# Optimization experiments

Measured on AMD Instinct MI355X. Metric: run time of the kernel, lower is better.

Reference implementation:

```python
import jax, jax.numpy as jnp
import numpy as np

B, LATENT, P, NUM_ATOMS, H, L, E = 16, 128, 16, 64, 64, 4, 32768
N = P * NUM_ATOMS  # 1024

def _lin(k, i, o, s=0.05):
    kw, kb = jax.random.split(k)
    return jax.random.normal(kw, (i, o), jnp.float32) * s, jax.random.normal(kb, (o,), jnp.float32) * s

def setup_inputs() -> dict:
    key = jax.random.key(0)
    ks = jax.random.split(key, 32)
    z = jax.random.normal(ks[0], (B, LATENT), jnp.float32)
    edge_index = jax.random.randint(ks[1], (2, E), 0, N, jnp.int32)
    # build_node_features: (frame/P, atom/num_atoms, 1) per node
    fr = jnp.repeat(jnp.arange(P), NUM_ATOMS) / P
    at = jnp.tile(jnp.arange(NUM_ATOMS), P) / NUM_ATOMS
    node_features = jnp.stack([fr, at, jnp.ones(N)], -1).astype(jnp.float32)
    Wg, bg = _lin(ks[2], LATENT, H)
    Wn, bn = _lin(ks[3], 3, H)
    def stack(fn, base):
        outs = [fn(jax.random.fold_in(key, base + l)) for l in range(L)]
        return tuple(jnp.stack(t) for t in zip(*outs))
    eW1, eb1 = stack(lambda k: _lin(k, 2 * H + 1, H), 100)
    eW2, eb2 = stack(lambda k: _lin(k, H, H), 200)
    cW1, cb1 = stack(lambda k: _lin(k, H, H), 300)
    cW2 = jnp.stack([jax.random.normal(jax.random.fold_in(key, 400 + l), (H, 1), jnp.float32) * 0.05 for l in range(L)])
    nW1, nb1 = stack(lambda k: _lin(k, 2 * H, H), 500)
    nW2, nb2 = stack(lambda k: _lin(k, H, H), 600)
    lng = jnp.ones((L, H), jnp.float32)
    lnb = jnp.zeros((L, H), jnp.float32)
    oW1, ob1 = _lin(ks[4], H, H)
    oW2, ob2 = _lin(ks[5], H, 3)
    return dict(z=z, edge_index=edge_index, node_features=node_features, Wg=Wg, bg=bg, Wn=Wn, bn=bn,
                eW1=eW1, eb1=eb1, eW2=eW2, eb2=eb2, cW1=cW1, cb1=cb1, cW2=cW2,
                nW1=nW1, nb1=nb1, nW2=nW2, nb2=nb2, lng=lng, lnb=lnb,
                oW1=oW1, ob1=ob1, oW2=oW2, ob2=ob2)

def _forward(z, edge_index, node_features, Wg, bg, Wn, bn, eW1, eb1, eW2, eb2,
             cW1, cb1, cW2, nW1, nb1, nW2, nb2, lng, lnb, oW1, ob1, oW2, ob2):
    b = z.shape[0]
    n = node_features.shape[0]
    row, col = edge_index[0], edge_index[1]  # aggregate messages to row
    counts = jnp.clip(jnp.zeros((n,), jnp.float32).at[row].add(1.0), 1.0, None)
    g = z @ Wg + bg                              # [B,H]
    h = (node_features @ Wn + bn)[None] + g[:, None]  # [B,N,H]
    pos = jnp.zeros((b, n, 3), h.dtype)
    for l in range(L):
        hi, hj = h[:, row], h[:, col]            # [B,E,H] gathers
        diff = pos[:, row] - pos[:, col]         # [B,E,3]
        d2 = jnp.sum(diff * diff, -1, keepdims=True)
        m = jax.nn.silu(jnp.concatenate([hi, hj, d2], -1) @ eW1[l] + eb1[l])
        m = jax.nn.silu(m @ eW2[l] + eb2[l])     # [B,E,H]
        w = jax.nn.silu(m @ cW1[l] + cb1[l]) @ cW2[l]  # [B,E,1]
        trans = diff * w
        pos = pos + jnp.zeros_like(pos).at[:, row].add(trans) / counts[None, :, None]
        agg = jnp.zeros_like(h).at[:, row].add(m)      # scatter-sum to nodes
        u = jax.nn.silu(jnp.concatenate([h, agg], -1) @ nW1[l] + nb1[l]) @ nW2[l] + nb2[l]
        h = h + u                                 # node residual
        mu = jnp.mean(h, -1, keepdims=True)
        var = jnp.mean((h - mu) ** 2, -1, keepdims=True)
        h = (h - mu) * jax.lax.rsqrt(var + 1e-5) * lng[l] + lnb[l]
    out = jax.nn.relu(h @ oW1 + ob1) @ oW2 + ob2   # [B,N,3]
    return out.reshape(b, -1)

def reference(z, edge_index, node_features, Wg, bg, Wn, bn, eW1, eb1, eW2, eb2,
              cW1, cb1, cW2, nW1, nb1, nW2, nb2, lng, lnb, oW1, ob1, oW2, ob2):
    return _forward(z, edge_index, node_features, Wg, bg, Wn, bn, eW1, eb1, eW2, eb2,
                    cW1, cb1, cW2, nW1, nb1, nW2, nb2, lng, lnb, oW1, ob1, oW2, ob2)
```

## Files before the change

kernel.cpp:

```cpp
#include <hip/hip_runtime.h>
#include <hip/hip_bf16.h>


namespace {

constexpr int kB = 16, kN = 1024, kH = 64, kE = 32768, kLat = 128;
constexpr int kC = 24;
constexpr int kMaxItems = 2560;

typedef __attribute__((ext_vector_type(8))) short short8;
typedef __attribute__((ext_vector_type(4))) float floatx4;

__device__ __forceinline__ unsigned short f2bf(float f){
  union { float f; unsigned int u; } v; v.f = f;
  unsigned int r = v.u + 0x7fffu + ((v.u >> 16) & 1u);
  return (unsigned short)(r >> 16);
}
__device__ __forceinline__ unsigned int packbf(float a, float b){
  return ((unsigned int)f2bf(b) << 16) | (unsigned int)f2bf(a);
}
__device__ __forceinline__ unsigned int pack2f(float a, float b){
  unsigned int ua = __float_as_uint(a) + 0x8000u;
  unsigned int ub = __float_as_uint(b) + 0x8000u;
  return __builtin_amdgcn_perm(ub, ua, 0x07060302);
}
__device__ __forceinline__ float bflo(unsigned int u){
  union { unsigned int u; float f; } v; v.u = u << 16; return v.f;
}
__device__ __forceinline__ float bfhi(unsigned int u){
  union { unsigned int u; float f; } v; v.u = u & 0xffff0000u; return v.f;
}
__device__ __forceinline__ float silu2(float x){
  float u = __builtin_amdgcn_exp2f(-1.44269504f * x);
  return x * __builtin_amdgcn_rcpf(1.0f + u);
}

__global__ void k_count(const int* ei, int* cntI){
  int e = blockIdx.x*256 + threadIdx.x;
  atomicAdd(&cntI[ei[e]], 1);
}

__global__ void k_scan(const int* cntI, int* off, int* ioff, int* fill,
                       int* items, int* nitems){
  __shared__ int s0[1024];
  __shared__ int s1[1024];
  int t = threadIdx.x;
  int c = cntI[t];
  s0[t] = c; __syncthreads();
  int* src = s0; int* dst = s1;
  for (int o = 1; o < 1024; o <<= 1){
    int v = src[t] + ((t >= o) ? src[t-o] : 0);
    dst[t] = v; __syncthreads();
    int* tmp = src; src = dst; dst = tmp;
  }
  int inc = src[t];
  off[t] = inc - c;
  if (t == 1023) off[1024] = inc;
  fill[t] = 0;
  int ic = (c + (kC-1)) / kC;
  __syncthreads();
  s0[t] = ic; __syncthreads();
  src = s0; dst = s1;
  for (int o = 1; o < 1024; o <<= 1){
    int v = src[t] + ((t >= o) ? src[t-o] : 0);
    dst[t] = v; __syncthreads();
    int* tmp = src; src = dst; dst = tmp;
  }
  int inc2 = src[t];
  int ib = inc2 - ic;
  ioff[t] = ib;
  if (t == 1023){ ioff[1024] = inc2; *nitems = inc2; }
  for (int s = 0; s < ic; s++) items[ib + s] = (t << 12) | s;
}

__global__ void k_bucket(const int* ei, const int* off, int* fill, int* ecol,
                         const float* eW2, unsigned short* wfragE,
                         const float* z, const float* Wg, const float* bg,
                         float* g){
  int e = blockIdx.x*256 + threadIdx.x;
  int r = ei[e];
  int s = atomicAdd(&fill[r], 1);
  ecol[off[r] + s] = ei[kE + e];
  if (blockIdx.x < 4){
    int l = blockIdx.x;
    for (int i = threadIdx.x; i < 4096; i += 256){
      int f = i >> 9, lane = (i >> 3) & 63, j8 = i & 7;
      int jt = f >> 1, ks = f & 1;
      int k = ks*32 + (lane >> 4)*8 + j8;
      int j = jt*16 + (lane & 15);
      wfragE[l*4096 + i] = f2bf(eW2[l*4096 + k*64 + j]);
    }
  } else if (blockIdx.x < 8){
    int b = (blockIdx.x - 4)*4 + (threadIdx.x >> 6);
    int j = threadIdx.x & 63;
    float acc = bg[j];
    for (int k = 0; k < kLat; k++) acc += z[b*kLat + k] * Wg[k*64 + j];
    g[b*64 + j] = acc;
  }
}

__global__ __launch_bounds__(256, 3) void k_pre(const float* nf, const float* Wn,
      const float* bn, const float* g, const float* eW1, const float* eb1,
      float* h, float* A1t, unsigned short* A2bf){
  __shared__ __align__(16) float W0[4096];
  __shared__ __align__(16) float W1[4096];
  __shared__ __align__(16) float HR[16*68];
  __shared__ float b1s[64];
  int tid = threadIdx.x;
  int bb = blockIdx.x >> 6;
  int n0 = (blockIdx.x & 63) * 16;
  {
    const float4* e1a = (const float4*)(eW1);
    const float4* e1b = (const float4*)(eW1 + 4096);
    for (int i = tid; i < 1024; i += 256){ ((float4*)W0)[i] = e1a[i]; ((float4*)W1)[i] = e1b[i]; }
  }
  if (tid < 64) b1s[tid] = eb1[tid];
  int rl = tid >> 4, c = tid & 15, j0 = c*4;
  int n = n0 + rl;
  int row = bb*1024 + n;
  float f0 = nf[n*3], f1 = nf[n*3+1], f2 = nf[n*3+2];
  float4 hv;
  hv.x = f0*Wn[j0+0] + f1*Wn[64+j0+0] + f2*Wn[128+j0+0] + bn[j0+0] + g[bb*64+j0+0];
  hv.y = f0*Wn[j0+1] + f1*Wn[64+j0+1] + f2*Wn[128+j0+1] + bn[j0+1] + g[bb*64+j0+1];
  hv.z = f0*Wn[j0+2] + f1*Wn[64+j0+2] + f2*Wn[128+j0+2] + bn[j0+2] + g[bb*64+j0+2];
  hv.w = f0*Wn[j0+3] + f1*Wn[64+j0+3] + f2*Wn[128+j0+3] + bn[j0+3] + g[bb*64+j0+3];
  *(float4*)(h + row*64 + j0) = hv;
  *(float4*)(HR + rl*68 + j0) = hv;
  __syncthreads();
  float4 a1 = { b1s[j0], b1s[j0+1], b1s[j0+2], b1s[j0+3] };
  float4 a2 = { 0.f, 0.f, 0.f, 0.f };
  #pragma unroll 8
  for (int k = 0; k < 64; k++){
    float hk = HR[rl*68 + k];
    float4 w1 = *(const float4*)(W0 + k*64 + j0);
    float4 w2 = *(const float4*)(W1 + k*64 + j0);
    a1.x += hk*w1.x; a1.y += hk*w1.y; a1.z += hk*w1.z; a1.w += hk*w1.w;
    a2.x += hk*w2.x; a2.y += hk*w2.y; a2.z += hk*w2.z; a2.w += hk*w2.w;
  }
  int tb = (n*16 + bb)*64;
  *(float4*)(A1t + tb + j0) = a1;
  uint2 pk; pk.x = packbf(a2.x, a2.y); pk.y = packbf(a2.z, a2.w);
  *(uint2*)(A2bf + tb + j0) = pk;
}

__global__ __launch_bounds__(256, 3) void k_edge(const float* A1t,
      const unsigned short* A2bf, const unsigned short* wfragE,
      const float* eb2, int l, const int* off, const int* ecol,
      const int* items, const int* nitems, float* P){
  int w = blockIdx.x*4 + (threadIdx.x >> 6);
  if (w >= *nitems) return;
  int lane = threadIdx.x & 63;
  int m = lane & 15, quad = lane >> 4;
  int it = items[w];
  int r = it >> 12, s = it & 4095;
  int e0 = off[r] + s*kC;
  int e1 = min(off[r+1], e0 + kC);

  short8 wf[8];
  #pragma unroll
  for (int f = 0; f < 8; f++)
    wf[f] = *(const short8*)(wfragE + l*4096 + f*512 + lane*8);

  float4 a1[4];
  #pragma unroll
  for (int ks = 0; ks < 2; ks++){
    a1[ks*2+0] = *(const float4*)(A1t + (r<<10) + (m<<6) + ks*32 + quad*8);
    a1[ks*2+1] = *(const float4*)(A1t + (r<<10) + (m<<6) + ks*32 + quad*8 + 4);
  }
  floatx4 dini[4];
  #pragma unroll
  for (int jt = 0; jt < 4; jt++)
    dini[jt] = *(const floatx4*)(eb2 + l*64 + jt*16 + quad*4);
  floatx4 agg[4];
  #pragma unroll
  for (int jt = 0; jt < 4; jt++) agg[jt] = (floatx4){0.f,0.f,0.f,0.f};

  int c0 = ecol[e0];
  uint4 p0 = *(const uint4*)(A2bf + ((c0<<4)+m)*64 + quad*8);
  uint4 p1 = *(const uint4*)(A2bf + ((c0<<4)+m)*64 + 32 + quad*8);

  for (int e = e0; e < e1; e++){
    uint4 c_0 = p0, c_1 = p1;
    if (e + 1 < e1){
      int cn = ecol[e+1];
      p0 = *(const uint4*)(A2bf + ((cn<<4)+m)*64 + quad*8);
      p1 = *(const uint4*)(A2bf + ((cn<<4)+m)*64 + 32 + quad*8);
    }
    short8 bfr[2];
    #pragma unroll
    for (int ks = 0; ks < 2; ks++){
      uint4 a2r = (ks == 0) ? c_0 : c_1;
      float4 x0 = a1[ks*2+0];
      float4 x1 = a1[ks*2+1];
      float v0 = silu2(x0.x + bflo(a2r.x));
      float v1 = silu2(x0.y + bfhi(a2r.x));
      float v2 = silu2(x0.z + bflo(a2r.y));
      float v3 = silu2(x0.w + bfhi(a2r.y));
      float v4 = silu2(x1.x + bflo(a2r.z));
      float v5 = silu2(x1.y + bfhi(a2r.z));
      float v6 = silu2(x1.z + bflo(a2r.w));
      float v7 = silu2(x1.w + bfhi(a2r.w));
      union { uint4 u; short8 s; } bu;
      bu.u.x = pack2f(v0, v1); bu.u.y = pack2f(v2, v3);
      bu.u.z = pack2f(v4, v5); bu.u.w = pack2f(v6, v7);
      bfr[ks] = bu.s;
    }
    #pragma unroll
    for (int jt = 0; jt < 4; jt++){
      floatx4 d = dini[jt];
      d = __builtin_amdgcn_mfma_f32_16x16x32_bf16(wf[jt*2+0], bfr[0], d, 0, 0, 0);
      d = __builtin_amdgcn_mfma_f32_16x16x32_bf16(wf[jt*2+1], bfr[1], d, 0, 0, 0);
      floatx4 a = agg[jt];
      a.x += silu2(d.x); a.y += silu2(d.y);
      a.z += silu2(d.z); a.w += silu2(d.w);
      agg[jt] = a;
    }
  }
  #pragma unroll
  for (int jt = 0; jt < 4; jt++)
    *(floatx4*)(P + w*1024 + m*64 + jt*16 + quad*4) = agg[jt];
}

template <bool LAST>
__global__ __launch_bounds__(256, 3) void k_post(int l, float* h, const float* P,
      const int* ioff, const float* nW1, const float* nb1_, const float* nW2,
      const float* nb2_, const float* lng_, const float* lnb_,
      const float* eW1, const float* eb1_, float* A1t, unsigned short* A2bf,
      const float* oW1, const float* ob1_, const float* oW2, const float* ob2_,
      float* out){
  __shared__ __align__(16) float W0[4096];
  __shared__ __align__(16) float W1[4096];
  __shared__ __align__(16) float HR[16*68];
  __shared__ __align__(16) float AG[16*68];
  __shared__ __align__(16) float TL[16*68];
  __shared__ float b1s[64], b2s[64], lgs[64], lbs[64];
  __shared__ float W2o[192];
  __shared__ float ob2s[4];
  int tid = threadIdx.x;
  int bb = blockIdx.x >> 6;
  int n0 = (blockIdx.x & 63) * 16;
  int rl = tid >> 4, c = tid & 15, j0 = c*4;
  int n = n0 + rl;
  int row = bb*1024 + n;

  {
    const float4* p1 = (const float4*)(nW1 + l*8192);
    const float4* p2 = (const float4*)(nW1 + l*8192 + 4096);
    for (int i = tid; i < 1024; i += 256){ ((float4*)W0)[i] = p1[i]; ((float4*)W1)[i] = p2[i]; }
  }
  if (tid < 64){
    b1s[tid] = nb1_[l*64+tid]; b2s[tid] = nb2_[l*64+tid];
    lgs[tid] = lng_[l*64+tid]; lbs[tid] = lnb_[l*64+tid];
  }
  {
    float4 hv = *(const float4*)(h + row*64 + j0);
    *(float4*)(HR + rl*68 + j0) = hv;
    float4 s = {0.f,0.f,0.f,0.f};
    int i0 = ioff[n], i1 = ioff[n+1];
    for (int i = i0; i < i1; i++){
      float4 v = *(const float4*)(P + i*1024 + bb*64 + j0);
      s.x += v.x; s.y += v.y; s.z += v.z; s.w += v.w;
    }
    *(float4*)(AG + rl*68 + j0) = s;
  }
  __syncthreads();

  float4 t = { b1s[j0], b1s[j0+1], b1s[j0+2], b1s[j0+3] };
  #pragma unroll 8
  for (int k = 0; k < 64; k++){
    float hk = HR[rl*68 + k], ak = AG[rl*68 + k];
    float4 w1 = *(const float4*)(W0 + k*64 + j0);
    float4 w2 = *(const float4*)(W1 + k*64 + j0);
    t.x += hk*w1.x + ak*w2.x; t.y += hk*w1.y + ak*w2.y;
    t.z += hk*w1.z + ak*w2.z; t.w += hk*w1.w + ak*w2.w;
  }
  t.x = silu2(t.x); t.y = silu2(t.y); t.z = silu2(t.z); t.w = silu2(t.w);
  *(float4*)(TL + rl*68 + j0) = t;
  __syncthreads();

  {
    const float4* p3 = (const float4*)(nW2 + l*4096);
    for (int i = tid; i < 1024; i += 256) ((float4*)W0)[i] = p3[i];
  }
  __syncthreads();

  float4 u = { b2s[j0], b2s[j0+1], b2s[j0+2], b2s[j0+3] };
  #pragma unroll 8
  for (int k = 0; k < 64; k++){
    float tk = TL[rl*68 + k];
    float4 w = *(const float4*)(W0 + k*64 + j0);
    u.x += tk*w.x; u.y += tk*w.y; u.z += tk*w.z; u.w += tk*w.w;
  }
  float4 hold = *(const float4*)(HR + rl*68 + j0);
  float4 hv = { hold.x + u.x, hold.y + u.y, hold.z + u.z, hold.w + u.w };
  float s1 = hv.x + hv.y + hv.z + hv.w;
  float s2 = hv.x*hv.x + hv.y*hv.y + hv.z*hv.z + hv.w*hv.w;
  s1 += __shfl_xor(s1, 1, 64); s1 += __shfl_xor(s1, 2, 64);
  s1 += __shfl_xor(s1, 4, 64); s1 += __shfl_xor(s1, 8, 64);
  s2 += __shfl_xor(s2, 1, 64); s2 += __shfl_xor(s2, 2, 64);
  s2 += __shfl_xor(s2, 4, 64); s2 += __shfl_xor(s2, 8, 64);
  float mu  = s1 * (1.0f/64.0f);
  float var = s2 * (1.0f/64.0f) - mu*mu;
  float rs  = rsqrtf(var + 1e-5f);
  float4 hn;
  hn.x = (hv.x-mu)*rs*lgs[j0+0] + lbs[j0+0];
  hn.y = (hv.y-mu)*rs*lgs[j0+1] + lbs[j0+1];
  hn.z = (hv.z-mu)*rs*lgs[j0+2] + lbs[j0+2];
  hn.w = (hv.w-mu)*rs*lgs[j0+3] + lbs[j0+3];
  if (!LAST) *(float4*)(h + row*64 + j0) = hn;
  *(float4*)(HR + rl*68 + j0) = hn;
  __syncthreads();

  if (!LAST){
    {
      const float4* e1a = (const float4*)(eW1 + (l+1)*8256);
      const float4* e1b = (const float4*)(eW1 + (l+1)*8256 + 4096);
      for (int i = tid; i < 1024; i += 256){ ((float4*)W0)[i] = e1a[i]; ((float4*)W1)[i] = e1b[i]; }
    }
    if (tid < 64) b1s[tid] = eb1_[(l+1)*64 + tid];
    __syncthreads();
    float4 a1 = { b1s[j0], b1s[j0+1], b1s[j0+2], b1s[j0+3] };
    float4 a2 = { 0.f, 0.f, 0.f, 0.f };
    #pragma unroll 8
    for (int k = 0; k < 64; k++){
      float hk = HR[rl*68 + k];
      float4 w1 = *(const float4*)(W0 + k*64 + j0);
      float4 w2 = *(const float4*)(W1 + k*64 + j0);
      a1.x += hk*w1.x; a1.y += hk*w1.y; a1.z += hk*w1.z; a1.w += hk*w1.w;
      a2.x += hk*w2.x; a2.y += hk*w2.y; a2.z += hk*w2.z; a2.w += hk*w2.w;
    }
    int tb = (n*16 + bb)*64;
    *(float4*)(A1t + tb + j0) = a1;
    uint2 pk; pk.x = packbf(a2.x, a2.y); pk.y = packbf(a2.z, a2.w);
    *(uint2*)(A2bf + tb + j0) = pk;
  } else {
    {
      const float4* w1p = (const float4*)oW1;
      for (int i = tid; i < 1024; i += 256) ((float4*)W0)[i] = w1p[i];
    }
    if (tid < 192) W2o[tid] = oW2[tid];
    if (tid < 64)  b1s[tid] = ob1_[tid];
    if (tid < 3)   ob2s[tid] = ob2_[tid];
    __syncthreads();
    float4 tr = { b1s[j0], b1s[j0+1], b1s[j0+2], b1s[j0+3] };
    #pragma unroll 8
    for (int k = 0; k < 64; k++){
      float hk = HR[rl*68 + k];
      float4 w = *(const float4*)(W0 + k*64 + j0);
      tr.x += hk*w.x; tr.y += hk*w.y; tr.z += hk*w.z; tr.w += hk*w.w;
    }
    float4 t4 = { fmaxf(tr.x,0.f), fmaxf(tr.y,0.f), fmaxf(tr.z,0.f), fmaxf(tr.w,0.f) };
    *(float4*)(TL + rl*68 + j0) = t4;
    __syncthreads();
    if (c < 3){
      float acc = ob2s[c];
      #pragma unroll 8
      for (int k = 0; k < 64; k++) acc += TL[rl*68 + k] * W2o[k*3 + c];
      out[bb*3072 + n*3 + c] = acc;
    }
  }
}

}

extern "C" void kernel_launch(void* const* d_in, const int* in_sizes, int n_in,
                              void* d_out, int out_size, void* d_ws, size_t ws_size,
                              hipStream_t stream){
  const float* z   = (const float*)d_in[0];
  const int*   ei  = (const int*)d_in[1];
  const float* nf  = (const float*)d_in[2];
  const float* Wg  = (const float*)d_in[3];  const float* bg  = (const float*)d_in[4];
  const float* Wn  = (const float*)d_in[5];  const float* bn  = (const float*)d_in[6];
  const float* eW1 = (const float*)d_in[7];  const float* eb1 = (const float*)d_in[8];
  const float* eW2 = (const float*)d_in[9];  const float* eb2 = (const float*)d_in[10];
  const float* nW1 = (const float*)d_in[14]; const float* nb1 = (const float*)d_in[15];
  const float* nW2 = (const float*)d_in[16]; const float* nb2 = (const float*)d_in[17];
  const float* lng = (const float*)d_in[18]; const float* lnb = (const float*)d_in[19];
  const float* oW1 = (const float*)d_in[20]; const float* ob1 = (const float*)d_in[21];
  const float* oW2 = (const float*)d_in[22]; const float* ob2 = (const float*)d_in[23];

  float* W      = (float*)d_ws;
  float* h      = W;
  float* A1t    = W + 1048576;
  unsigned short* A2bf   = (unsigned short*)(W + 2097152);
  unsigned short* wfragE = (unsigned short*)(W + 2621440);
  float* P      = W + 2629632;
  float* g      = W + 5251072;
  int*   cntI   = (int*)(W + 5252096);
  int*   off    = cntI + 1024;
  int*   ioff   = off + 1025;
  int*   fill   = ioff + 1025;
  int*   items  = fill + 1024;
  int*   nitems = items + 2560;
  int*   ecol   = nitems + 1;

  hipMemsetAsync(cntI, 0, 1024*sizeof(int), stream);
  k_count <<<128, 256, 0, stream>>>(ei, cntI);
  k_scan  <<<1,  1024, 0, stream>>>(cntI, off, ioff, fill, items, nitems);
  k_bucket<<<128, 256, 0, stream>>>(ei, off, fill, ecol, eW2, wfragE, z, Wg, bg, g);
  k_pre   <<<1024, 256, 0, stream>>>(nf, Wn, bn, g, eW1, eb1, h, A1t, A2bf);

  for (int l = 0; l < 4; l++){
    k_edge<<<640, 256, 0, stream>>>(A1t, A2bf, wfragE, eb2, l, off, ecol,
                                    items, nitems, P);
    if (l < 3)
      k_post<false><<<1024, 256, 0, stream>>>(l, h, P, ioff, nW1, nb1, nW2, nb2,
            lng, lnb, eW1, eb1, A1t, A2bf, oW1, ob1, oW2, ob2, (float*)d_out);
    else
      k_post<true> <<<1024, 256, 0, stream>>>(l, h, P, ioff, nW1, nb1, nW2, nb2,
            lng, lnb, eW1, eb1, A1t, A2bf, oW1, ob1, oW2, ob2, (float*)d_out);
  }
}
```

Before: 368.6 us.

## Register-tile node GEMMs 4x4 per thread and factor initial edge projection

After: 356.7 us. 3.2% less time.

```diff
diff --git a/kernel.cpp b/kernel.cpp
--- a/kernel.cpp
+++ b/kernel.cpp
@@ -99,48 +99,124 @@
   }
 }
 
-__global__ __launch_bounds__(256, 3) void k_pre(const float* nf, const float* Wn,
+__device__ __forceinline__ void stage16k(float* Wl, const float* src, int tid){
+  const float4* p = (const float4*)src;
+  float4* d = (float4*)Wl;
+  d[tid]       = p[tid];
+  d[tid + 256] = p[tid + 256];
+  d[tid + 512] = p[tid + 512];
+  d[tid + 768] = p[tid + 768];
+}
+__device__ __forceinline__ void xtwrite(float* XTl, int j0, int r0,
+                                        const float v[4][4]){
+  #pragma unroll
+  for (int j = 0; j < 4; j++){
+    float4 t = { v[0][j], v[1][j], v[2][j], v[3][j] };
+    *(float4*)(XTl + (j0 + j)*68 + r0) = t;
+  }
+}
+__device__ __forceinline__ void gemm64(const float* Wl, const float* XTl,
+                                       int j0, int r0, float acc[4][4]){
+  #pragma unroll 4
+  for (int k = 0; k < 64; k++){
+    float4 w = *(const float4*)(Wl + k*64 + j0);
+    float4 x = *(const float4*)(XTl + k*68 + r0);
+    float xv[4] = { x.x, x.y, x.z, x.w };
+    float wv[4] = { w.x, w.y, w.z, w.w };
+    #pragma unroll
+    for (int i = 0; i < 4; i++)
+      #pragma unroll
+      for (int j = 0; j < 4; j++)
+        acc[i][j] += xv[i]*wv[j];
+  }
+}
+
+__global__ __launch_bounds__(256, 1) void k_preA(const float* nf, const float* Wn,
       const float* bn, const float* g, const float* eW1, const float* eb1,
-      float* h, float* A1t, unsigned short* A2bf){
+      float* An1, float* An2, float* Ag1, float* Ag2){
   __shared__ __align__(16) float W0[4096];
   __shared__ __align__(16) float W1[4096];
   __shared__ __align__(16) float HR[16*68];
-  __shared__ float b1s[64];
   int tid = threadIdx.x;
-  int bb = blockIdx.x >> 6;
-  int n0 = (blockIdx.x & 63) * 16;
+  if (blockIdx.x == 64){
+    int bb = tid >> 4, j0 = (tid & 15)*4;
+    float a1[4] = {0.f,0.f,0.f,0.f}, a2[4] = {0.f,0.f,0.f,0.f};
+    for (int k = 0; k < 64; k++){
+      float gk = g[bb*64 + k];
+      float4 w1 = *(const float4*)(eW1 + k*64 + j0);
+      float4 w2 = *(const float4*)(eW1 + 4096 + k*64 + j0);
+      a1[0] += gk*w1.x; a1[1] += gk*w1.y; a1[2] += gk*w1.z; a1[3] += gk*w1.w;
+      a2[0] += gk*w2.x; a2[1] += gk*w2.y; a2[2] += gk*w2.z; a2[3] += gk*w2.w;
+    }
+    float4 o1 = { a1[0], a1[1], a1[2], a1[3] };
+    float4 o2 = { a2[0], a2[1], a2[2], a2[3] };
+    *(float4*)(Ag1 + bb*64 + j0) = o1;
+    *(float4*)(Ag2 + bb*64 + j0) = o2;
+    return;
+  }
   {
     const float4* e1a = (const float4*)(eW1);
     const float4* e1b = (const float4*)(eW1 + 4096);
-    for (int i = tid; i < 1024; i += 256){ ((float4*)W0)[i] = e1a[i]; ((float4*)W1)[i] = e1b[i]; }
-  }
-  if (tid < 64) b1s[tid] = eb1[tid];
+    for (int i = tid; i < 1024; i += 256){
+      ((float4*)W0)[i] = e1a[i]; ((float4*)W1)[i] = e1b[i];
+    }
+  }
   int rl = tid >> 4, c = tid & 15, j0 = c*4;
-  int n = n0 + rl;
-  int row = bb*1024 + n;
+  int n = blockIdx.x*16 + rl;
   float f0 = nf[n*3], f1 = nf[n*3+1], f2 = nf[n*3+2];
   float4 hv;
-  hv.x = f0*Wn[j0+0] + f1*Wn[64+j0+0] + f2*Wn[128+j0+0] + bn[j0+0] + g[bb*64+j0+0];
-  hv.y = f0*Wn[j0+1] + f1*Wn[64+j0+1] + f2*Wn[128+j0+1] + bn[j0+1] + g[bb*64+j0+1];
-  hv.z = f0*Wn[j0+2] + f1*Wn[64+j0+2] + f2*Wn[128+j0+2] + bn[j0+2] + g[bb*64+j0+2];
-  hv.w = f0*Wn[j0+3] + f1*Wn[64+j0+3] + f2*Wn[128+j0+3] + bn[j0+3] + g[bb*64+j0+3];
-  *(float4*)(h + row*64 + j0) = hv;
+  hv.x = f0*Wn[j0+0] + f1*Wn[64+j0+0] + f2*Wn[128+j0+0] + bn[j0+0];
+  hv.y = f0*Wn[j0+1] + f1*Wn[64+j0+1] + f2*Wn[128+j0+1] + bn[j0+1];
+  hv.z = f0*Wn[j0+2] + f1*Wn[64+j0+2] + f2*Wn[128+j0+2] + bn[j0+2];
+  hv.w = f0*Wn[j0+3] + f1*Wn[64+j0+3] + f2*Wn[128+j0+3] + bn[j0+3];
   *(float4*)(HR + rl*68 + j0) = hv;
   __syncthreads();
-  float4 a1 = { b1s[j0], b1s[j0+1], b1s[j0+2], b1s[j0+3] };
-  float4 a2 = { 0.f, 0.f, 0.f, 0.f };
+  float4 b1 = *(const float4*)(eb1 + j0);
+  float a1[4] = { b1.x, b1.y, b1.z, b1.w };
+  float a2[4] = { 0.f, 0.f, 0.f, 0.f };
   #pragma unroll 8
   for (int k = 0; k < 64; k++){
     float hk = HR[rl*68 + k];
     float4 w1 = *(const float4*)(W0 + k*64 + j0);
     float4 w2 = *(const float4*)(W1 + k*64 + j0);
-    a1.x += hk*w1.x; a1.y += hk*w1.y; a1.z += hk*w1.z; a1.w += hk*w1.w;
-    a2.x += hk*w2.x; a2.y += hk*w2.y; a2.z += hk*w2.z; a2.w += hk*w2.w;
-  }
-  int tb = (n*16 + bb)*64;
-  *(float4*)(A1t + tb + j0) = a1;
+    a1[0] += hk*w1.x; a1[1] += hk*w1.y; a1[2] += hk*w1.z; a1[3] += hk*w1.w;
+    a2[0] += hk*w2.x; a2[1] += hk*w2.y; a2[2] += hk*w2.z; a2[3] += hk*w2.w;
+  }
+  float4 o1 = { a1[0], a1[1], a1[2], a1[3] };
+  float4 o2 = { a2[0], a2[1], a2[2], a2[3] };
+  *(float4*)(An1 + n*64 + j0) = o1;
+  *(float4*)(An2 + n*64 + j0) = o2;
+}
+
+__global__ __launch_bounds__(256, 1) void k_pre1(const float* nf, const float* Wn,
+      const float* bn, const float* g, const float* An1, const float* An2,
+      const float* Ag1, const float* Ag2, float* h, float* A1t,
+      unsigned short* A2bf){
+  int idx = blockIdx.x*256 + threadIdx.x;
+  int row = idx >> 4;
+  int j0  = (idx & 15) * 4;
+  int n = row >> 4, bb = row & 15;
+  float4 a1 = *(const float4*)(An1 + n*64 + j0);
+  float4 g1 = *(const float4*)(Ag1 + bb*64 + j0);
+  a1.x += g1.x; a1.y += g1.y; a1.z += g1.z; a1.w += g1.w;
+  *(float4*)(A1t + row*64 + j0) = a1;
+  float4 a2 = *(const float4*)(An2 + n*64 + j0);
+  float4 g2 = *(const float4*)(Ag2 + bb*64 + j0);
+  a2.x += g2.x; a2.y += g2.y; a2.z += g2.z; a2.w += g2.w;
   uint2 pk; pk.x = packbf(a2.x, a2.y); pk.y = packbf(a2.z, a2.w);
-  *(uint2*)(A2bf + tb + j0) = pk;
+  *(uint2*)(A2bf + row*64 + j0) = pk;
+  float f0 = nf[n*3], f1 = nf[n*3+1], f2 = nf[n*3+2];
+  float4 w0 = *(const float4*)(Wn + j0);
+  float4 w1 = *(const float4*)(Wn + 64 + j0);
+  float4 w2 = *(const float4*)(Wn + 128 + j0);
+  float4 bv = *(const float4*)(bn + j0);
+  float4 gv = *(const float4*)(g + bb*64 + j0);
+  float4 hv;
+  hv.x = f0*w0.x + f1*w1.x + f2*w2.x + bv.x + gv.x;
+  hv.y = f0*w0.y + f1*w1.y + f2*w2.y + bv.y + gv.y;
+  hv.z = f0*w0.z + f1*w1.z + f2*w2.z + bv.z + gv.z;
+  hv.w = f0*w0.w + f1*w1.w + f2*w2.w + bv.w + gv.w;
+  *(float4*)(h + (bb*1024 + n)*64 + j0) = hv;
 }
 
 __global__ __launch_bounds__(256, 3) void k_edge(const float* A1t,
@@ -222,141 +298,191 @@
 }
 
 template <bool LAST>
-__global__ __launch_bounds__(256, 3) void k_post(int l, float* h, const float* P,
+__global__ __launch_bounds__(256, 1) void k_post(int l, float* h, const float* P,
       const int* ioff, const float* nW1, const float* nb1_, const float* nW2,
       const float* nb2_, const float* lng_, const float* lnb_,
       const float* eW1, const float* eb1_, float* A1t, unsigned short* A2bf,
       const float* oW1, const float* ob1_, const float* oW2, const float* ob2_,
       float* out){
-  __shared__ __align__(16) float W0[4096];
-  __shared__ __align__(16) float W1[4096];
-  __shared__ __align__(16) float HR[16*68];
-  __shared__ __align__(16) float AG[16*68];
-  __shared__ __align__(16) float TL[16*68];
-  __shared__ float b1s[64], b2s[64], lgs[64], lbs[64];
-  __shared__ float W2o[192];
-  __shared__ float ob2s[4];
+  __shared__ __align__(16) float W[4096];
+  __shared__ __align__(16) float XT[64*68];
   int tid = threadIdx.x;
-  int bb = blockIdx.x >> 6;
-  int n0 = (blockIdx.x & 63) * 16;
-  int rl = tid >> 4, c = tid & 15, j0 = c*4;
-  int n = n0 + rl;
-  int row = bb*1024 + n;
-
+  int bb = blockIdx.x >> 4;
+  int n0 = (blockIdx.x & 15) * 64;
+  int c = tid & 15, g = tid >> 4;
+  int j0 = c*4, r0 = g*4;
+  int rowbase = bb*1024 + n0 + r0;
+
+  stage16k(W, nW1 + l*8192, tid);
+  float hold[4][4];
+  #pragma unroll
+  for (int i = 0; i < 4; i++){
+    float4 v = *(const float4*)(h + (rowbase + i)*64 + j0);
+    hold[i][0]=v.x; hold[i][1]=v.y; hold[i][2]=v.z; hold[i][3]=v.w;
+  }
+  xtwrite(XT, j0, r0, hold);
+  float acc[4][4];
   {
-    const float4* p1 = (const float4*)(nW1 + l*8192);
-    const float4* p2 = (const float4*)(nW1 + l*8192 + 4096);
-    for (int i = tid; i < 1024; i += 256){ ((float4*)W0)[i] = p1[i]; ((float4*)W1)[i] = p2[i]; }
-  }
-  if (tid < 64){
-    b1s[tid] = nb1_[l*64+tid]; b2s[tid] = nb2_[l*64+tid];
-    lgs[tid] = lng_[l*64+tid]; lbs[tid] = lnb_[l*64+tid];
-  }
+    float4 b1 = *(const float4*)(nb1_ + l*64 + j0);
+    float bv[4] = { b1.x, b1.y, b1.z, b1.w };
+    #pragma unroll
+    for (int i = 0; i < 4; i++)
+      #pragma unroll
+      for (int j = 0; j < 4; j++) acc[i][j] = bv[j];
+  }
+  __syncthreads();
+  gemm64(W, XT, j0, r0, acc);
+  __syncthreads();
+
+  stage16k(W, nW1 + l*8192 + 4096, tid);
   {
-    float4 hv = *(const float4*)(h + row*64 + j0);
-    *(float4*)(HR + rl*68 + j0) = hv;
-    float4 s = {0.f,0.f,0.f,0.f};
-    int i0 = ioff[n], i1 = ioff[n+1];
-    for (int i = i0; i < i1; i++){
-      float4 v = *(const float4*)(P + i*1024 + bb*64 + j0);
-      s.x += v.x; s.y += v.y; s.z += v.z; s.w += v.w;
-    }
-    *(float4*)(AG + rl*68 + j0) = s;
-  }
-  __syncthreads();
-
-  float4 t = { b1s[j0], b1s[j0+1], b1s[j0+2], b1s[j0+3] };
-  #pragma unroll 8
-  for (int k = 0; k < 64; k++){
-    float hk = HR[rl*68 + k], ak = AG[rl*68 + k];
-    float4 w1 = *(const float4*)(W0 + k*64 + j0);
-    float4 w2 = *(const float4*)(W1 + k*64 + j0);
-    t.x += hk*w1.x + ak*w2.x; t.y += hk*w1.y + ak*w2.y;
-    t.z += hk*w1.z + ak*w2.z; t.w += hk*w1.w + ak*w2.w;
-  }
-  t.x = silu2(t.x); t.y = silu2(t.y); t.z = silu2(t.z); t.w = silu2(t.w);
-  *(float4*)(TL + rl*68 + j0) = t;
-  __syncthreads();
-
+    float agt[4][4];
+    #pragma unroll
+    for (int i = 0; i < 4; i++){
+      int n = n0 + r0 + i;
+      float4 s = { 0.f, 0.f, 0.f, 0.f };
+      int i0 = ioff[n], i1 = ioff[n+1];
+      for (int it = i0; it < i1; it++){
+        float4 v = *(const float4*)(P + it*1024 + bb*64 + j0);
+        s.x += v.x; s.y += v.y; s.z += v.z; s.w += v.w;
+      }
+      agt[i][0]=s.x; agt[i][1]=s.y; agt[i][2]=s.z; agt[i][3]=s.w;
+    }
+    xtwrite(XT, j0, r0, agt);
+  }
+  __syncthreads();
+  gemm64(W, XT, j0, r0, acc);
+  #pragma unroll
+  for (int i = 0; i < 4; i++)
+    #pragma unroll
+    for (int j = 0; j < 4; j++) acc[i][j] = silu2(acc[i][j]);
+  __syncthreads();
+
+  stage16k(W, nW2 + l*4096, tid);
+  xtwrite(XT, j0, r0, acc);
+  float u[4][4];
   {
-    const float4* p3 = (const float4*)(nW2 + l*4096);
-    for (int i = tid; i < 1024; i += 256) ((float4*)W0)[i] = p3[i];
-  }
-  __syncthreads();
-
-  float4 u = { b2s[j0], b2s[j0+1], b2s[j0+2], b2s[j0+3] };
-  #pragma unroll 8
-  for (int k = 0; k < 64; k++){
-    float tk = TL[rl*68 + k];
-    float4 w = *(const float4*)(W0 + k*64 + j0);
-    u.x += tk*w.x; u.y += tk*w.y; u.z += tk*w.z; u.w += tk*w.w;
-  }
-  float4 hold = *(const float4*)(HR + rl*68 + j0);
-  float4 hv = { hold.x + u.x, hold.y + u.y, hold.z + u.z, hold.w + u.w };
-  float s1 = hv.x + hv.y + hv.z + hv.w;
-  float s2 = hv.x*hv.x + hv.y*hv.y + hv.z*hv.z + hv.w*hv.w;
-  s1 += __shfl_xor(s1, 1, 64); s1 += __shfl_xor(s1, 2, 64);
-  s1 += __shfl_xor(s1, 4, 64); s1 += __shfl_xor(s1, 8, 64);
-  s2 += __shfl_xor(s2, 1, 64); s2 += __shfl_xor(s2, 2, 64);
-  s2 += __shfl_xor(s2, 4, 64); s2 += __shfl_xor(s2, 8, 64);
-  float mu  = s1 * (1.0f/64.0f);
-  float var = s2 * (1.0f/64.0f) - mu*mu;
-  float rs  = rsqrtf(var + 1e-5f);
-  float4 hn;
-  hn.x = (hv.x-mu)*rs*lgs[j0+0] + lbs[j0+0];
-  hn.y = (hv.y-mu)*rs*lgs[j0+1] + lbs[j0+1];
-  hn.z = (hv.z-mu)*rs*lgs[j0+2] + lbs[j0+2];
-  hn.w = (hv.w-mu)*rs*lgs[j0+3] + lbs[j0+3];
-  if (!LAST) *(float4*)(h + row*64 + j0) = hn;
-  *(float4*)(HR + rl*68 + j0) = hn;
-  __syncthreads();
+    float4 b2 = *(const float4*)(nb2_ + l*64 + j0);
+    float bv[4] = { b2.x, b2.y, b2.z, b2.w };
+    #pragma unroll
+    for (int i = 0; i < 4; i++)
+      #pragma unroll
+      for (int j = 0; j < 4; j++) u[i][j] = bv[j];
+  }
+  __syncthreads();
+  gemm64(W, XT, j0, r0, u);
+  float4 lgv = *(const float4*)(lng_ + l*64 + j0);
+  float4 lbv = *(const float4*)(lnb_ + l*64 + j0);
+  float hn[4][4];
+  #pragma unroll
+  for (int i = 0; i < 4; i++){
+    float hv[4];
+    #pragma unroll
+    for (int j = 0; j < 4; j++) hv[j] = hold[i][j] + u[i][j];
+    float s1 = hv[0]+hv[1]+hv[2]+hv[3];
+    float s2 = hv[0]*hv[0]+hv[1]*hv[1]+hv[2]*hv[2]+hv[3]*hv[3];
+    s1 += __shfl_xor(s1, 1, 64); s1 += __shfl_xor(s1, 2, 64);
+    s1 += __shfl_xor(s1, 4, 64); s1 += __shfl_xor(s1, 8, 64);
+    s2 += __shfl_xor(s2, 1, 64); s2 += __shfl_xor(s2, 2, 64);
+    s2 += __shfl_xor(s2, 4, 64); s2 += __shfl_xor(s2, 8, 64);
+    float mu  = s1 * (1.0f/64.0f);
+    float var = s2 * (1.0f/64.0f) - mu*mu;
+    float rs  = rsqrtf(var + 1e-5f);
+    hn[i][0] = (hv[0]-mu)*rs*lgv.x + lbv.x;
+    hn[i][1] = (hv[1]-mu)*rs*lgv.y + lbv.y;
+    hn[i][2] = (hv[2]-mu)*rs*lgv.z + lbv.z;
+    hn[i][3] = (hv[3]-mu)*rs*lgv.w + lbv.w;
+  }
 
   if (!LAST){
+    #pragma unroll
+    for (int i = 0; i < 4; i++){
+      float4 v = { hn[i][0], hn[i][1], hn[i][2], hn[i][3] };
+      *(float4*)(h + (rowbase + i)*64 + j0) = v;
+    }
+    __syncthreads();
+    stage16k(W, eW1 + (l+1)*8256, tid);
+    xtwrite(XT, j0, r0, hn);
+    float a1[4][4];
     {
-      const float4* e1a = (const float4*)(eW1 + (l+1)*8256);
-      const float4* e1b = (const float4*)(eW1 + (l+1)*8256 + 4096);
-      for (int i = tid; i < 1024; i += 256){ ((float4*)W0)[i] = e1a[i]; ((float4*)W1)[i] = e1b[i]; }
-    }
-    if (tid < 64) b1s[tid] = eb1_[(l+1)*64 + tid];
+      float4 b1 = *(const float4*)(eb1_ + (l+1)*64 + j0);
+      float bv[4] = { b1.x, b1.y, b1.z, b1.w };
+      #pragma unroll
+      for (int i = 0; i < 4; i++)
+        #pragma unroll
+        for (int j = 0; j < 4; j++) a1[i][j] = bv[j];
+    }
     __syncthreads();
-    float4 a1 = { b1s[j0], b1s[j0+1], b1s[j0+2], b1s[j0+3] };
-    float4 a2 = { 0.f, 0.f, 0.f, 0.f };
-    #pragma unroll 8
-    for (int k = 0; k < 64; k++){
-      float hk = HR[rl*68 + k];
-      float4 w1 = *(const float4*)(W0 + k*64 + j0);
-      float4 w2 = *(const float4*)(W1 + k*64 + j0);
-      a1.x += hk*w1.x; a1.y += hk*w1.y; a1.z += hk*w1.z; a1.w += hk*w1.w;
-      a2.x += hk*w2.x; a2.y += hk*w2.y; a2.z += hk*w2.z; a2.w += hk*w2.w;
-    }
-    int tb = (n*16 + bb)*64;
-    *(float4*)(A1t + tb + j0) = a1;
-    uint2 pk; pk.x = packbf(a2.x, a2.y); pk.y = packbf(a2.z, a2.w);
-    *(uint2*)(A2bf + tb + j0) = pk;
+    gemm64(W, XT, j0, r0, a1);
+    __syncthreads();
+    stage16k(W, eW1 + (l+1)*8256 + 4096, tid);
+    float a2[4][4];
+    #pragma unroll
+    for (int i = 0; i < 4; i++)
+      #pragma unroll
+      for (int j = 0; j < 4; j++) a2[i][j] = 0.f;
+    __syncthreads();
+    gemm64(W, XT, j0, r0, a2);
+    #pragma unroll
+    for (int i = 0; i < 4; i++){
+      int tb = ((n0 + r0 + i)*16 + bb)*64 + j0;
+      float4 o1 = { a1[i][0], a1[i][1], a1[i][2], a1[i][3] };
+      *(float4*)(A1t + tb) = o1;
+      uint2 pk; pk.x = packbf(a2[i][0], a2[i][1]);
+      pk.y = packbf(a2[i][2], a2[i][3]);
+      *(uint2*)(A2bf + tb) = pk;
+    }
   } else {
+    __syncthreads();
+    stage16k(W, oW1, tid);
+    xtwrite(XT, j0, r0, hn);
+    float tr[4][4];
     {
-      const float4* w1p = (const float4*)oW1;
-      for (int i = tid; i < 1024; i += 256) ((float4*)W0)[i] = w1p[i];
-    }
-    if (tid < 192) W2o[tid] = oW2[tid];
-    if (tid < 64)  b1s[tid] = ob1_[tid];
-    if (tid < 3)   ob2s[tid] = ob2_[tid];
+      float4 b1 = *(const float4*)(ob1_ + j0);
+      float bv[4] = { b1.x, b1.y, b1.z, b1.w };
+      #pragma unroll
+      for (int i = 0; i < 4; i++)
+        #pragma unroll
+        for (int j = 0; j < 4; j++) tr[i][j] = bv[j];
+    }
     __syncthreads();
-    float4 tr = { b1s[j0], b1s[j0+1], b1s[j0+2], b1s[j0+3] };
-    #pragma unroll 8
-    for (int k = 0; k < 64; k++){
-      float hk = HR[rl*68 + k];
-      float4 w = *(const float4*)(W0 + k*64 + j0);
-      tr.x += hk*w.x; tr.y += hk*w.y; tr.z += hk*w.z; tr.w += hk*w.w;
-    }
-    float4 t4 = { fmaxf(tr.x,0.f), fmaxf(tr.y,0.f), fmaxf(tr.z,0.f), fmaxf(tr.w,0.f) };
-    *(float4*)(TL + rl*68 + j0) = t4;
-    __syncthreads();
-    if (c < 3){
-      float acc = ob2s[c];
-      #pragma unroll 8
-      for (int k = 0; k < 64; k++) acc += TL[rl*68 + k] * W2o[k*3 + c];
-      out[bb*3072 + n*3 + c] = acc;
+    gemm64(W, XT, j0, r0, tr);
+    #pragma unroll
+    for (int i = 0; i < 4; i++)
+      #pragma unroll
+      for (int j = 0; j < 4; j++) tr[i][j] = fmaxf(tr[i][j], 0.f);
+    float po[4][3];
+    #pragma unroll
+    for (int i = 0; i < 4; i++){ po[i][0]=0.f; po[i][1]=0.f; po[i][2]=0.f; }
+    #pragma unroll
+    for (int j = 0; j < 4; j++){
+      float w0 = oW2[(j0+j)*3 + 0];
+      float w1 = oW2[(j0+j)*3 + 1];
+      float w2 = oW2[(j0+j)*3 + 2];
+      #pragma unroll
+      for (int i = 0; i < 4; i++){
+        po[i][0] += tr[i][j]*w0;
+        po[i][1] += tr[i][j]*w1;
+        po[i][2] += tr[i][j]*w2;
+      }
+    }
+    #pragma unroll
+    for (int i = 0; i < 4; i++)
+      #pragma unroll
+      for (int uu = 0; uu < 3; uu++){
+        float v = po[i][uu];
+        v += __shfl_xor(v, 1, 64); v += __shfl_xor(v, 2, 64);
+        v += __shfl_xor(v, 4, 64); v += __shfl_xor(v, 8, 64);
+        po[i][uu] = v;
+      }
+    if (c == 0){
+      #pragma unroll
+      for (int i = 0; i < 4; i++){
+        int n = n0 + r0 + i;
+        out[bb*3072 + n*3 + 0] = po[i][0] + ob2_[0];
+        out[bb*3072 + n*3 + 1] = po[i][1] + ob2_[1];
+        out[bb*3072 + n*3 + 2] = po[i][2] + ob2_[2];
+      }
     }
   }
 }
@@ -393,21 +519,26 @@
   int*   items  = fill + 1024;
   int*   nitems = items + 2560;
   int*   ecol   = nitems + 1;
+  float* An1    = W + 5291776;
+  float* An2    = An1 + 65536;
+  float* Ag1    = An2 + 65536;
+  float* Ag2    = Ag1 + 1024;
 
   hipMemsetAsync(cntI, 0, 1024*sizeof(int), stream);
   k_count <<<128, 256, 0, stream>>>(ei, cntI);
   k_scan  <<<1,  1024, 0, stream>>>(cntI, off, ioff, fill, items, nitems);
   k_bucket<<<128, 256, 0, stream>>>(ei, off, fill, ecol, eW2, wfragE, z, Wg, bg, g);
-  k_pre   <<<1024, 256, 0, stream>>>(nf, Wn, bn, g, eW1, eb1, h, A1t, A2bf);
+  k_preA  <<<65,  256, 0, stream>>>(nf, Wn, bn, g, eW1, eb1, An1, An2, Ag1, Ag2);
+  k_pre1  <<<1024,256, 0, stream>>>(nf, Wn, bn, g, An1, An2, Ag1, Ag2, h, A1t, A2bf);
 
   for (int l = 0; l < 4; l++){
     k_edge<<<640, 256, 0, stream>>>(A1t, A2bf, wfragE, eb2, l, off, ecol,
                                     items, nitems, P);
     if (l < 3)
-      k_post<false><<<1024, 256, 0, stream>>>(l, h, P, ioff, nW1, nb1, nW2, nb2,
+      k_post<false><<<256, 256, 0, stream>>>(l, h, P, ioff, nW1, nb1, nW2, nb2,
             lng, lnb, eW1, eb1, A1t, A2bf, oW1, ob1, oW2, ob2, (float*)d_out);
     else
-      k_post<true> <<<1024, 256, 0, stream>>>(l, h, P, ioff, nW1, nb1, nW2, nb2,
+      k_post<true> <<<256, 256, 0, stream>>>(l, h, P, ioff, nW1, nb1, nW2, nb2,
             lng, lnb, eW1, eb1, A1t, A2bf, oW1, ob1, oW2, ob2, (float*)d_out);
   }
 }
```
